# Kernel tuning notes

Hardware: AMD Instinct MI355X
Metric: run time of the kernel (lower is better)

## Reference

```python
import jax, jax.numpy as jnp
import numpy as np

MAX_WORDS = 2048  # max word tokens per sequence (static num_segments)


def setup_inputs() -> dict:
    key = jax.random.key(0)
    k1, k2, k3, k4 = jax.random.split(key, 4)
    B, S, H, D = 8, 4096, 768, 1024
    embeddings = jax.random.normal(k1, (B, S, H), dtype=jnp.float32)
    proj_w = jax.random.normal(k2, (H, D), dtype=jnp.float32) * 0.02
    proj_b = jax.random.normal(k3, (D,), dtype=jnp.float32) * 0.02
    masks = jnp.ones((B, S), dtype=jnp.int32)
    word_ids = jnp.sort(jax.random.randint(k4, (B, S), 0, MAX_WORDS), axis=-1)
    return {"embeddings": embeddings, "proj_w": proj_w, "proj_b": proj_b,
            "masks": masks, "word_ids": word_ids}


def reference(embeddings, proj_w, proj_b, masks, word_ids):
    B, S, H = embeddings.shape
    W = MAX_WORDS
    # Flatten batch+word into one segment id space: seg in [0, B*W)
    seg = (word_ids + jnp.arange(B, dtype=word_ids.dtype)[:, None] * W).reshape(-1)
    flat_emb = embeddings.reshape(B * S, H)
    # segment-sum of embeddings over subwords of each word  -> (B, W, H)
    sum_emb = jax.ops.segment_sum(flat_emb, seg, num_segments=B * W).reshape(B, W, H)
    ones = jnp.ones((B * S,), dtype=jnp.float32)
    counts = jax.ops.segment_sum(ones, seg, num_segments=B * W).reshape(B, W)
    mcounts = jax.ops.segment_sum(masks.reshape(-1).astype(jnp.float32), seg,
                                  num_segments=B * W).reshape(B, W)
    # word is valid iff it has >=1 subword and ALL its subwords have mask==1
    valid = (counts > 0) & (counts == mcounts)
    mean_emb = sum_emb / jnp.maximum(counts, 1.0)[..., None]
    token_embeddings = jnp.where(valid[..., None], mean_emb, 0.0)  # (B, W, H)
    token_masks = valid.astype(jnp.int32)                          # (B, W)
    # projection: hidden 768 -> config.hidden_size 1024
    out = jnp.einsum('bwh,hd->bwd', token_embeddings, proj_w) + proj_b
    return out, token_masks
```

## Files before the change

kernel.cpp:

```cpp
#include <hip/hip_runtime.h>
#include <hip/hip_bf16.h>
#include <stdint.h>

#define Bn 8
#define Sn 4096
#define Hn 768
#define Dn 1024
#define Wn 2048

typedef __attribute__((ext_vector_type(8))) short short8;
typedef __attribute__((ext_vector_type(4))) short short4v;
typedef __attribute__((ext_vector_type(4))) float floatx4;

__device__ __forceinline__ void load_lds16(const void* g, void* l) {
  __builtin_amdgcn_global_load_lds(
      (const __attribute__((address_space(1))) void*)g,
      (__attribute__((address_space(3))) void*)l, 16, 0, 0);
}

__global__ __launch_bounds__(256) void k_prep(const float* __restrict__ pw,
                                              const int* __restrict__ wid,
                                              __hip_bfloat16* __restrict__ wb,
                                              int* __restrict__ starts) {
  if (blockIdx.x < 768) {
    __shared__ float tile[32][33];
    const int bt = blockIdx.x;
    const int d0 = (bt % 32) * 32, h0 = (bt / 32) * 32;
    const int tx = threadIdx.x & 31, ty = threadIdx.x >> 5;
#pragma unroll
    for (int i = 0; i < 32; i += 8)
      tile[ty + i][tx] = pw[(size_t)(h0 + ty + i) * Dn + d0 + tx];
    __syncthreads();
#pragma unroll
    for (int i = 0; i < 32; i += 8)
      wb[(size_t)(d0 + ty + i) * Hn + h0 + tx] = (__hip_bfloat16)tile[tx][ty + i];
  } else {
    const int bid = blockIdx.x - 768;
    const int g = bid * 256 + threadIdx.x;
    const int b = g >> 12, s = g & (Sn - 1);
    const int* wbi = wid + (size_t)b * Sn;
    int* sb = starts + b * (Wn + 1);
    const int cur = wbi[s];
    const int prev = (s == 0) ? -1 : wbi[s - 1];
    for (int ww = prev + 1; ww <= cur; ++ww) sb[ww] = s;
    if (s == Sn - 1)
      for (int ww = cur + 1; ww <= Wn; ++ww) sb[ww] = Sn;
  }
}

__global__ __launch_bounds__(256) void k_words(const float* __restrict__ emb,
                                               const int* __restrict__ masks,
                                               const int* __restrict__ starts,
                                               __hip_bfloat16* __restrict__ wa,
                                               float* __restrict__ out_masks) {
  const int b = blockIdx.y;
  const int wave = threadIdx.x >> 6, lane = threadIdx.x & 63;
  const int w = blockIdx.x * 4 + wave;

  const int* sb = starts + b * (Wn + 1);
  const int start = sb[w];
  const int end = sb[w + 1];
  const int count = end - start;

  const int* mb = masks + (size_t)b * Sn;
  bool allone = true;
  for (int s0 = start; s0 < end; s0 += 64) {
    const int idx = s0 + lane;
    allone = allone && ((idx < end) ? (mb[idx] == 1) : true);
  }
  const bool valid = (count > 0) && __all(allone);
  const float inv = valid ? 1.0f / (float)count : 0.0f;

  floatx4 sum[3] = {{0.f, 0.f, 0.f, 0.f}, {0.f, 0.f, 0.f, 0.f}, {0.f, 0.f, 0.f, 0.f}};
  const float* eb = emb + (size_t)b * Sn * Hn;
  int s = start;
  for (; s + 1 < end; s += 2) {
    const floatx4* r0 = (const floatx4*)(eb + (size_t)s * Hn);
    const floatx4* r1 = (const floatx4*)(eb + (size_t)(s + 1) * Hn);
#pragma unroll
    for (int j = 0; j < 3; ++j) sum[j] += r0[j * 64 + lane];
#pragma unroll
    for (int j = 0; j < 3; ++j) sum[j] += r1[j * 64 + lane];
  }
  if (s < end) {
    const floatx4* r0 = (const floatx4*)(eb + (size_t)s * Hn);
#pragma unroll
    for (int j = 0; j < 3; ++j) sum[j] += r0[j * 64 + lane];
  }

  const size_t rowbase = ((size_t)b * Wn + w) * Hn;
#pragma unroll
  for (int j = 0; j < 3; ++j) {
    short4v o;
#pragma unroll
    for (int c = 0; c < 4; ++c) {
      __hip_bfloat16 h = (__hip_bfloat16)(sum[j][c] * inv);
      o[c] = *reinterpret_cast<short*>(&h);
    }
    *(short4v*)&wa[rowbase + (size_t)(j * 64 + lane) * 4] = o;
  }
  if (lane == 0) out_masks[(size_t)b * Wn + w] = valid ? 1.0f : 0.0f;
}

constexpr int GK = Hn;
constexpr int LDS_A = 256 * 64;
constexpr int LDS_B = 128 * 64;
constexpr int LDS_T = LDS_A + LDS_B;

__global__ __launch_bounds__(512, 2) void k_gemm(const short* __restrict__ A,
                                                 const short* __restrict__ Bt,
                                                 const float* __restrict__ bias,
                                                 float* __restrict__ out) {
  extern __shared__ __align__(16) short ls[];

  const int t = threadIdx.x;
  const int lane = t & 63;
  const int wave = t >> 6;
  const int wm = wave >> 1, wn = wave & 1;
  const int lane16 = lane & 15, quad = lane >> 4;
  const int swz = lane16 & 7;

  const int linear = blockIdx.x;
  const int xcd = linear & 7;
  const int o = linear >> 3;
  const int m0 = (xcd * 8 + (o >> 3)) * 256;
  const int n0 = (o & 7) * 128;

  const int rA = t >> 3;
  const int ssw = ((t & 7) ^ (rA & 7)) * 8;
  const short* gAs = A + (size_t)(m0 + rA) * GK + ssw;
  const short* gBs = Bt + (size_t)(n0 + rA) * GK + ssw;

  auto stage_a3 = [&](int slot, int tt) {
    short* d = ls + slot * LDS_T + t * 8;
    const short* g = gAs + tt * 64;
    load_lds16(g, d);
    load_lds16(g + (size_t)64 * GK, d + 4096);
    load_lds16(g + (size_t)128 * GK, d + 8192);
  };
  auto stage_b3 = [&](int slot, int tt) {
    short* d = ls + slot * LDS_T + t * 8;
    load_lds16(gAs + tt * 64 + (size_t)192 * GK, d + 12288);
    load_lds16(gBs + tt * 64, d + 16384);
    load_lds16(gBs + tt * 64 + (size_t)64 * GK, d + 20480);
  };

  auto ld_af = [&](short8 (&af)[2][2], int mib, const short* bufA) {
#pragma unroll
    for (int m2 = 0; m2 < 2; ++m2)
#pragma unroll
      for (int ks = 0; ks < 2; ++ks)
        af[m2][ks] = *(const short8*)&bufA[(wm * 64 + (mib + m2) * 16 + lane16) * 64 +
                                           ((((ks << 2) | quad) ^ swz) << 3)];
  };
  auto ld_bf = [&](short8 (&bf)[4][2], const short* bufB) {
#pragma unroll
    for (int ni = 0; ni < 4; ++ni)
#pragma unroll
      for (int ks = 0; ks < 2; ++ks)
        bf[ni][ks] = *(const short8*)&bufB[(wn * 64 + ni * 16 + lane16) * 64 +
                                           ((((ks << 2) | quad) ^ swz) << 3)];
  };

  floatx4 acc[4][4];
#pragma unroll
  for (int i = 0; i < 4; ++i)
#pragma unroll
    for (int j = 0; j < 4; ++j) acc[i][j] = (floatx4){0.f, 0.f, 0.f, 0.f};

  auto mmac2 = [&](short8 (&af)[2][2], short8 (&bf)[4][2], int mib) {
    __builtin_amdgcn_s_setprio(1);
#pragma unroll
    for (int m2 = 0; m2 < 2; ++m2)
#pragma unroll
      for (int ni = 0; ni < 4; ++ni)
#pragma unroll
        for (int ks = 0; ks < 2; ++ks)
          acc[mib + m2][ni] = __builtin_amdgcn_mfma_f32_16x16x32_bf16(
              af[m2][ks], bf[ni][ks], acc[mib + m2][ni], 0, 0, 0);
    __builtin_amdgcn_s_setprio(0);
  };

  stage_a3(0, 0);
  stage_b3(0, 0);
  stage_a3(1, 1);
  stage_b3(1, 1);
  asm volatile("s_waitcnt vmcnt(6)" ::: "memory");
  __builtin_amdgcn_sched_barrier(0);
  __builtin_amdgcn_s_barrier();

  int cur = 0;
#pragma unroll 1
  for (int tt = 0; tt < 12; ++tt) {
    const short* bufA = ls + cur * LDS_T;
    const short* bufB = bufA + LDS_A;
    const int nx2 = (cur + 2 >= 3) ? cur - 1 : cur + 2;
    const bool st = tt < 10;
    short8 af[2][2], bf[4][2];

    ld_af(af, 0, bufA);
    ld_bf(bf, bufB);
    if (st) stage_a3(nx2, tt + 2);
    __builtin_amdgcn_s_barrier();
    asm volatile("s_waitcnt lgkmcnt(0)" ::: "memory");
    __builtin_amdgcn_sched_barrier(0);
    mmac2(af, bf, 0);
    __builtin_amdgcn_s_barrier();

    ld_af(af, 2, bufA);
    if (st) stage_b3(nx2, tt + 2);
    if (tt < 10) {
      asm volatile("s_waitcnt vmcnt(6)" ::: "memory");
    } else if (tt == 10) {
      asm volatile("s_waitcnt vmcnt(0)" ::: "memory");
    }
    __builtin_amdgcn_sched_barrier(0);
    __builtin_amdgcn_s_barrier();
    asm volatile("s_waitcnt lgkmcnt(0)" ::: "memory");
    __builtin_amdgcn_sched_barrier(0);
    mmac2(af, bf, 2);
    __builtin_amdgcn_s_barrier();

    cur = (cur + 1 == 3) ? 0 : cur + 1;
  }

  float bv[4];
#pragma unroll
  for (int ni = 0; ni < 4; ++ni) bv[ni] = bias[n0 + wn * 64 + ni * 16 + lane16];

#pragma unroll
  for (int mi = 0; mi < 4; ++mi) {
#pragma unroll
    for (int ni = 0; ni < 4; ++ni) {
      const int n = n0 + wn * 64 + ni * 16 + lane16;
#pragma unroll
      for (int r = 0; r < 4; ++r) {
        const int m = m0 + wm * 64 + mi * 16 + quad * 4 + r;
        out[(size_t)m * Dn + n] = acc[mi][ni][r] + bv[ni];
      }
    }
  }
}

extern "C" void kernel_launch(void* const* d_in, const int* in_sizes, int n_in,
                              void* d_out, int out_size, void* d_ws, size_t ws_size,
                              hipStream_t stream) {
  const float* emb    = (const float*)d_in[0];
  const float* proj_w = (const float*)d_in[1];
  const float* proj_b = (const float*)d_in[2];
  const int*   masks  = (const int*)d_in[3];
  const int*   wid    = (const int*)d_in[4];

  float* out = (float*)d_out;
  float* out_masks = out + (size_t)Bn * Wn * Dn;

  __hip_bfloat16* wb = (__hip_bfloat16*)d_ws;
  __hip_bfloat16* wa = wb + (size_t)Dn * Hn;
  int* starts = (int*)(wa + (size_t)Bn * Wn * Hn);

  k_prep<<<dim3(768 + (Bn * Sn) / 256), 256, 0, stream>>>(proj_w, wid, wb, starts);

  k_words<<<dim3(Wn / 4, Bn), 256, 0, stream>>>(emb, masks, starts, wa, out_masks);

  constexpr int kGemmLds = 3 * LDS_T * (int)sizeof(short);
  static_assert(kGemmLds == 147456, "LDS budget");
  (void)hipFuncSetAttribute((const void*)k_gemm,
                            hipFuncAttributeMaxDynamicSharedMemorySize, kGemmLds);
  k_gemm<<<dim3(512), 512, kGemmLds, stream>>>((const short*)wa, (const short*)wb,
                                               proj_b, out);
}
```

Baseline: 209.9 us.

## Fuse prep, word pooling and GEMM into one cooperative persistent kernel

```diff
diff --git a/kernel.cpp b/kernel.cpp
--- a/kernel.cpp
+++ b/kernel.cpp
@@ -1,6 +1,9 @@
 #include <hip/hip_runtime.h>
+#include <hip/hip_cooperative_groups.h>
 #include <hip/hip_bf16.h>
 #include <stdint.h>
+
+namespace cg = cooperative_groups;
 
 #define Bn 8
 #define Sn 4096
@@ -12,31 +15,47 @@
 typedef __attribute__((ext_vector_type(4))) short short4v;
 typedef __attribute__((ext_vector_type(4))) float floatx4;
 
+constexpr int GK = Hn;
+constexpr int LDS_A = 256 * 64;
+constexpr int LDS_B = 128 * 64;
+constexpr int LDS_T = LDS_A + LDS_B;
+constexpr int kLdsBytes = 3 * LDS_T * (int)sizeof(short);
+static_assert(kLdsBytes == 147456, "LDS budget");
+
 __device__ __forceinline__ void load_lds16(const void* g, void* l) {
   __builtin_amdgcn_global_load_lds(
       (const __attribute__((address_space(1))) void*)g,
       (__attribute__((address_space(3))) void*)l, 16, 0, 0);
 }
 
-__global__ __launch_bounds__(256) void k_prep(const float* __restrict__ pw,
-                                              const int* __restrict__ wid,
-                                              __hip_bfloat16* __restrict__ wb,
-                                              int* __restrict__ starts) {
-  if (blockIdx.x < 768) {
-    __shared__ float tile[32][33];
-    const int bt = blockIdx.x;
-    const int d0 = (bt % 32) * 32, h0 = (bt / 32) * 32;
-    const int tx = threadIdx.x & 31, ty = threadIdx.x >> 5;
-#pragma unroll
-    for (int i = 0; i < 32; i += 8)
-      tile[ty + i][tx] = pw[(size_t)(h0 + ty + i) * Dn + d0 + tx];
-    __syncthreads();
-#pragma unroll
-    for (int i = 0; i < 32; i += 8)
-      wb[(size_t)(d0 + ty + i) * Hn + h0 + tx] = (__hip_bfloat16)tile[tx][ty + i];
+__global__ __launch_bounds__(512, 2) void k_fused(
+    const float* __restrict__ emb, const float* __restrict__ pw,
+    const float* __restrict__ bias, const int* __restrict__ masks,
+    const int* __restrict__ wid, short* wb, short* wa, int* starts,
+    float* __restrict__ out, float* __restrict__ out_masks) {
+  extern __shared__ __align__(16) short ls[];
+  const int t = threadIdx.x;
+  const int bid = blockIdx.x;
+  cg::grid_group grid = cg::this_grid();
+
+  if (bid < 192) {
+    float* tile = (float*)ls;
+    const int tx = t & 31, ty = t >> 5;
+#pragma unroll 1
+    for (int i = 0; i < 4; ++i) {
+      const int bt = bid * 4 + i;
+      const int d0 = (bt & 31) * 32, h0 = (bt >> 5) * 32;
+      tile[ty * 33 + tx] = pw[(size_t)(h0 + ty) * Dn + d0 + tx];
+      tile[(ty + 16) * 33 + tx] = pw[(size_t)(h0 + ty + 16) * Dn + d0 + tx];
+      __syncthreads();
+      __hip_bfloat16 v0 = (__hip_bfloat16)tile[tx * 33 + ty];
+      __hip_bfloat16 v1 = (__hip_bfloat16)tile[tx * 33 + ty + 16];
+      wb[(size_t)(d0 + ty) * Hn + h0 + tx] = *(short*)&v0;
+      wb[(size_t)(d0 + ty + 16) * Hn + h0 + tx] = *(short*)&v1;
+      __syncthreads();
+    }
   } else {
-    const int bid = blockIdx.x - 768;
-    const int g = bid * 256 + threadIdx.x;
+    const int g = (bid - 192) * 512 + t;
     const int b = g >> 12, s = g & (Sn - 1);
     const int* wbi = wid + (size_t)b * Sn;
     int* sb = starts + b * (Wn + 1);
@@ -46,197 +65,197 @@
     if (s == Sn - 1)
       for (int ww = cur + 1; ww <= Wn; ++ww) sb[ww] = Sn;
   }
-}
-
-__global__ __launch_bounds__(256) void k_words(const float* __restrict__ emb,
-                                               const int* __restrict__ masks,
-                                               const int* __restrict__ starts,
-                                               __hip_bfloat16* __restrict__ wa,
-                                               float* __restrict__ out_masks) {
-  const int b = blockIdx.y;
-  const int wave = threadIdx.x >> 6, lane = threadIdx.x & 63;
-  const int w = blockIdx.x * 4 + wave;
-
-  const int* sb = starts + b * (Wn + 1);
-  const int start = sb[w];
-  const int end = sb[w + 1];
-  const int count = end - start;
-
-  const int* mb = masks + (size_t)b * Sn;
-  bool allone = true;
-  for (int s0 = start; s0 < end; s0 += 64) {
-    const int idx = s0 + lane;
-    allone = allone && ((idx < end) ? (mb[idx] == 1) : true);
+  __threadfence();
+  grid.sync();
+
+  {
+    const int wave = t >> 6, lane = t & 63;
+    const int gw0 = (bid * 8 + wave) * 8;
+    const int b = gw0 >> 11;
+    const int w0 = gw0 & (Wn - 1);
+    const int* sb = starts + b * (Wn + 1);
+    const int pre = (lane < 9) ? sb[w0 + lane] : 0;
+    const int* mb = masks + (size_t)b * Sn;
+    const float* eb = emb + (size_t)b * Sn * Hn;
+
+    for (int wi = 0; wi < 8; ++wi) {
+      const int start = __shfl(pre, wi);
+      const int end = __shfl(pre, wi + 1);
+      const int count = end - start;
+
+      bool allone = true;
+      for (int s0 = start; s0 < end; s0 += 64) {
+        const int idx = s0 + lane;
+        allone = allone && ((idx < end) ? (mb[idx] == 1) : true);
+      }
+      const bool valid = (count > 0) && __all(allone);
+      const float inv = valid ? 1.0f / (float)count : 0.0f;
+
+      floatx4 sum[3] = {{0.f, 0.f, 0.f, 0.f}, {0.f, 0.f, 0.f, 0.f},
+                        {0.f, 0.f, 0.f, 0.f}};
+      int s = start;
+      for (; s + 1 < end; s += 2) {
+        const floatx4* r0 = (const floatx4*)(eb + (size_t)s * Hn);
+        const floatx4* r1 = (const floatx4*)(eb + (size_t)(s + 1) * Hn);
+#pragma unroll
+        for (int j = 0; j < 3; ++j) sum[j] += r0[j * 64 + lane];
+#pragma unroll
+        for (int j = 0; j < 3; ++j) sum[j] += r1[j * 64 + lane];
+      }
+      if (s < end) {
+        const floatx4* r0 = (const floatx4*)(eb + (size_t)s * Hn);
+#pragma unroll
+        for (int j = 0; j < 3; ++j) sum[j] += r0[j * 64 + lane];
+      }
+
+      const int w = w0 + wi;
+      const size_t rowbase = ((size_t)b * Wn + w) * Hn;
+#pragma unroll
+      for (int j = 0; j < 3; ++j) {
+        short4v o;
+#pragma unroll
+        for (int c = 0; c < 4; ++c) {
+          __hip_bfloat16 h = (__hip_bfloat16)(sum[j][c] * inv);
+          o[c] = *reinterpret_cast<short*>(&h);
+        }
+        *(short4v*)&wa[rowbase + (size_t)(j * 64 + lane) * 4] = o;
+      }
+      if (lane == 0) out_masks[(size_t)b * Wn + w] = valid ? 1.0f : 0.0f;
+    }
   }
-  const bool valid = (count > 0) && __all(allone);
-  const float inv = valid ? 1.0f / (float)count : 0.0f;
-
-  floatx4 sum[3] = {{0.f, 0.f, 0.f, 0.f}, {0.f, 0.f, 0.f, 0.f}, {0.f, 0.f, 0.f, 0.f}};
-  const float* eb = emb + (size_t)b * Sn * Hn;
-  int s = start;
-  for (; s + 1 < end; s += 2) {
-    const floatx4* r0 = (const floatx4*)(eb + (size_t)s * Hn);
-    const floatx4* r1 = (const floatx4*)(eb + (size_t)(s + 1) * Hn);
-#pragma unroll
-    for (int j = 0; j < 3; ++j) sum[j] += r0[j * 64 + lane];
-#pragma unroll
-    for (int j = 0; j < 3; ++j) sum[j] += r1[j * 64 + lane];
-  }
-  if (s < end) {
-    const floatx4* r0 = (const floatx4*)(eb + (size_t)s * Hn);
-#pragma unroll
-    for (int j = 0; j < 3; ++j) sum[j] += r0[j * 64 + lane];
-  }
-
-  const size_t rowbase = ((size_t)b * Wn + w) * Hn;
-#pragma unroll
-  for (int j = 0; j < 3; ++j) {
-    short4v o;
-#pragma unroll
-    for (int c = 0; c < 4; ++c) {
-      __hip_bfloat16 h = (__hip_bfloat16)(sum[j][c] * inv);
-      o[c] = *reinterpret_cast<short*>(&h);
-    }
-    *(short4v*)&wa[rowbase + (size_t)(j * 64 + lane) * 4] = o;
-  }
-  if (lane == 0) out_masks[(size_t)b * Wn + w] = valid ? 1.0f : 0.0f;
-}
-
-constexpr int GK = Hn;
-constexpr int LDS_A = 256 * 64;
-constexpr int LDS_B = 128 * 64;
-constexpr int LDS_T = LDS_A + LDS_B;
-
-__global__ __launch_bounds__(512, 2) void k_gemm(const short* __restrict__ A,
-                                                 const short* __restrict__ Bt,
-                                                 const float* __restrict__ bias,
-                                                 float* __restrict__ out) {
-  extern __shared__ __align__(16) short ls[];
-
-  const int t = threadIdx.x;
-  const int lane = t & 63;
-  const int wave = t >> 6;
-  const int wm = wave >> 1, wn = wave & 1;
-  const int lane16 = lane & 15, quad = lane >> 4;
-  const int swz = lane16 & 7;
-
-  const int linear = blockIdx.x;
-  const int xcd = linear & 7;
-  const int o = linear >> 3;
-  const int m0 = (xcd * 8 + (o >> 3)) * 256;
-  const int n0 = (o & 7) * 128;
-
-  const int rA = t >> 3;
-  const int ssw = ((t & 7) ^ (rA & 7)) * 8;
-  const short* gAs = A + (size_t)(m0 + rA) * GK + ssw;
-  const short* gBs = Bt + (size_t)(n0 + rA) * GK + ssw;
-
-  auto stage_a3 = [&](int slot, int tt) {
-    short* d = ls + slot * LDS_T + t * 8;
-    const short* g = gAs + tt * 64;
-    load_lds16(g, d);
-    load_lds16(g + (size_t)64 * GK, d + 4096);
-    load_lds16(g + (size_t)128 * GK, d + 8192);
-  };
-  auto stage_b3 = [&](int slot, int tt) {
-    short* d = ls + slot * LDS_T + t * 8;
-    load_lds16(gAs + tt * 64 + (size_t)192 * GK, d + 12288);
-    load_lds16(gBs + tt * 64, d + 16384);
-    load_lds16(gBs + tt * 64 + (size_t)64 * GK, d + 20480);
-  };
-
-  auto ld_af = [&](short8 (&af)[2][2], int mib, const short* bufA) {
-#pragma unroll
-    for (int m2 = 0; m2 < 2; ++m2)
-#pragma unroll
-      for (int ks = 0; ks < 2; ++ks)
-        af[m2][ks] = *(const short8*)&bufA[(wm * 64 + (mib + m2) * 16 + lane16) * 64 +
-                                           ((((ks << 2) | quad) ^ swz) << 3)];
-  };
-  auto ld_bf = [&](short8 (&bf)[4][2], const short* bufB) {
-#pragma unroll
-    for (int ni = 0; ni < 4; ++ni)
-#pragma unroll
-      for (int ks = 0; ks < 2; ++ks)
-        bf[ni][ks] = *(const short8*)&bufB[(wn * 64 + ni * 16 + lane16) * 64 +
-                                           ((((ks << 2) | quad) ^ swz) << 3)];
-  };
-
-  floatx4 acc[4][4];
-#pragma unroll
-  for (int i = 0; i < 4; ++i)
-#pragma unroll
-    for (int j = 0; j < 4; ++j) acc[i][j] = (floatx4){0.f, 0.f, 0.f, 0.f};
-
-  auto mmac2 = [&](short8 (&af)[2][2], short8 (&bf)[4][2], int mib) {
-    __builtin_amdgcn_s_setprio(1);
-#pragma unroll
-    for (int m2 = 0; m2 < 2; ++m2)
+  __threadfence();
+  grid.sync();
+
+  {
+    const int lane = t & 63, wave = t >> 6;
+    const int wm = wave >> 1, wn = wave & 1;
+    const int lane16 = lane & 15, quad = lane >> 4;
+    const int swz = lane16 & 7;
+
+    const int xcd = bid & 7, o = bid >> 3;
+    const int m0 = (xcd * 8 + (o >> 2)) * 256;
+    const int n0b = (o & 3) * 256;
+
+    const int rA = t >> 3;
+    const int ssw = ((t & 7) ^ (rA & 7)) * 8;
+    const short* gAs = (const short*)wa + (size_t)(m0 + rA) * GK + ssw;
+
+#pragma unroll 1
+    for (int nt = 0; nt < 2; ++nt) {
+      const int n0 = n0b + nt * 128;
+      const short* gBs = (const short*)wb + (size_t)(n0 + rA) * GK + ssw;
+
+      auto stage_a3 = [&](int slot, int tt) {
+        short* d = ls + slot * LDS_T + t * 8;
+        const short* g = gAs + tt * 64;
+        load_lds16(g, d);
+        load_lds16(g + (size_t)64 * GK, d + 4096);
+        load_lds16(g + (size_t)128 * GK, d + 8192);
+      };
+      auto stage_b3 = [&](int slot, int tt) {
+        short* d = ls + slot * LDS_T + t * 8;
+        load_lds16(gAs + tt * 64 + (size_t)192 * GK, d + 12288);
+        load_lds16(gBs + tt * 64, d + 16384);
+        load_lds16(gBs + tt * 64 + (size_t)64 * GK, d + 20480);
+      };
+      auto ld_af = [&](short8(&af)[2][2], int mib, const short* bufA) {
+#pragma unroll
+        for (int m2 = 0; m2 < 2; ++m2)
+#pragma unroll
+          for (int ks = 0; ks < 2; ++ks)
+            af[m2][ks] = *(const short8*)&bufA[(wm * 64 + (mib + m2) * 16 + lane16) * 64 +
+                                               ((((ks << 2) | quad) ^ swz) << 3)];
+      };
+      auto ld_bf = [&](short8(&bf)[4][2], const short* bufB) {
+#pragma unroll
+        for (int ni = 0; ni < 4; ++ni)
+#pragma unroll
+          for (int ks = 0; ks < 2; ++ks)
+            bf[ni][ks] = *(const short8*)&bufB[(wn * 64 + ni * 16 + lane16) * 64 +
+                                               ((((ks << 2) | quad) ^ swz) << 3)];
+      };
+
+      floatx4 acc[4][4];
+#pragma unroll
+      for (int i = 0; i < 4; ++i)
+#pragma unroll
+        for (int j = 0; j < 4; ++j) acc[i][j] = (floatx4){0.f, 0.f, 0.f, 0.f};
+
+      auto mmac2 = [&](short8(&af)[2][2], short8(&bf)[4][2], int mib) {
+        __builtin_amdgcn_s_setprio(1);
+#pragma unroll
+        for (int m2 = 0; m2 < 2; ++m2)
+#pragma unroll
+          for (int ni = 0; ni < 4; ++ni)
+#pragma unroll
+            for (int ks = 0; ks < 2; ++ks)
+              acc[mib + m2][ni] = __builtin_amdgcn_mfma_f32_16x16x32_bf16(
+                  af[m2][ks], bf[ni][ks], acc[mib + m2][ni], 0, 0, 0);
+        __builtin_amdgcn_s_setprio(0);
+      };
+
+      asm volatile("s_waitcnt vmcnt(0)" ::: "memory");
+      __builtin_amdgcn_sched_barrier(0);
+
+      stage_a3(0, 0);
+      stage_b3(0, 0);
+      stage_a3(1, 1);
+      stage_b3(1, 1);
+      asm volatile("s_waitcnt vmcnt(6)" ::: "memory");
+      __builtin_amdgcn_sched_barrier(0);
+      __builtin_amdgcn_s_barrier();
+
+      int cur = 0;
+#pragma unroll 1
+      for (int tt = 0; tt < 12; ++tt) {
+        const short* bufA = ls + cur * LDS_T;
+        const short* bufB = bufA + LDS_A;
+        const int nx2 = (cur + 2 >= 3) ? cur - 1 : cur + 2;
+        const bool st = tt < 10;
+        short8 af[2][2], bf[4][2];
+
+        ld_af(af, 0, bufA);
+        ld_bf(bf, bufB);
+        if (st) stage_a3(nx2, tt + 2);
+        __builtin_amdgcn_s_barrier();
+        asm volatile("s_waitcnt lgkmcnt(0)" ::: "memory");
+        __builtin_amdgcn_sched_barrier(0);
+        mmac2(af, bf, 0);
+        __builtin_amdgcn_s_barrier();
+
+        ld_af(af, 2, bufA);
+        if (st) stage_b3(nx2, tt + 2);
+        if (tt < 10) {
+          asm volatile("s_waitcnt vmcnt(6)" ::: "memory");
+        } else if (tt == 10) {
+          asm volatile("s_waitcnt vmcnt(0)" ::: "memory");
+        }
+        __builtin_amdgcn_sched_barrier(0);
+        __builtin_amdgcn_s_barrier();
+        asm volatile("s_waitcnt lgkmcnt(0)" ::: "memory");
+        __builtin_amdgcn_sched_barrier(0);
+        mmac2(af, bf, 2);
+        __builtin_amdgcn_s_barrier();
+
+        cur = (cur + 1 == 3) ? 0 : cur + 1;
+      }
+
+      float bv[4];
 #pragma unroll
       for (int ni = 0; ni < 4; ++ni)
-#pragma unroll
-        for (int ks = 0; ks < 2; ++ks)
-          acc[mib + m2][ni] = __builtin_amdgcn_mfma_f32_16x16x32_bf16(
-              af[m2][ks], bf[ni][ks], acc[mib + m2][ni], 0, 0, 0);
-    __builtin_amdgcn_s_setprio(0);
-  };
-
-  stage_a3(0, 0);
-  stage_b3(0, 0);
-  stage_a3(1, 1);
-  stage_b3(1, 1);
-  asm volatile("s_waitcnt vmcnt(6)" ::: "memory");
-  __builtin_amdgcn_sched_barrier(0);
-  __builtin_amdgcn_s_barrier();
-
-  int cur = 0;
-#pragma unroll 1
-  for (int tt = 0; tt < 12; ++tt) {
-    const short* bufA = ls + cur * LDS_T;
-    const short* bufB = bufA + LDS_A;
-    const int nx2 = (cur + 2 >= 3) ? cur - 1 : cur + 2;
-    const bool st = tt < 10;
-    short8 af[2][2], bf[4][2];
-
-    ld_af(af, 0, bufA);
-    ld_bf(bf, bufB);
-    if (st) stage_a3(nx2, tt + 2);
-    __builtin_amdgcn_s_barrier();
-    asm volatile("s_waitcnt lgkmcnt(0)" ::: "memory");
-    __builtin_amdgcn_sched_barrier(0);
-    mmac2(af, bf, 0);
-    __builtin_amdgcn_s_barrier();
-
-    ld_af(af, 2, bufA);
-    if (st) stage_b3(nx2, tt + 2);
-    if (tt < 10) {
-      asm volatile("s_waitcnt vmcnt(6)" ::: "memory");
-    } else if (tt == 10) {
-      asm volatile("s_waitcnt vmcnt(0)" ::: "memory");
-    }
-    __builtin_amdgcn_sched_barrier(0);
-    __builtin_amdgcn_s_barrier();
-    asm volatile("s_waitcnt lgkmcnt(0)" ::: "memory");
-    __builtin_amdgcn_sched_barrier(0);
-    mmac2(af, bf, 2);
-    __builtin_amdgcn_s_barrier();
-
-    cur = (cur + 1 == 3) ? 0 : cur + 1;
-  }
-
-  float bv[4];
-#pragma unroll
-  for (int ni = 0; ni < 4; ++ni) bv[ni] = bias[n0 + wn * 64 + ni * 16 + lane16];
-
-#pragma unroll
-  for (int mi = 0; mi < 4; ++mi) {
-#pragma unroll
-    for (int ni = 0; ni < 4; ++ni) {
-      const int n = n0 + wn * 64 + ni * 16 + lane16;
-#pragma unroll
-      for (int r = 0; r < 4; ++r) {
-        const int m = m0 + wm * 64 + mi * 16 + quad * 4 + r;
-        out[(size_t)m * Dn + n] = acc[mi][ni][r] + bv[ni];
+        bv[ni] = bias[n0 + wn * 64 + ni * 16 + lane16];
+
+#pragma unroll
+      for (int mi = 0; mi < 4; ++mi) {
+#pragma unroll
+        for (int ni = 0; ni < 4; ++ni) {
+          const int n = n0 + wn * 64 + ni * 16 + lane16;
+#pragma unroll
+          for (int r = 0; r < 4; ++r) {
+            const int m = m0 + wm * 64 + mi * 16 + quad * 4 + r;
+            out[(size_t)m * Dn + n] = acc[mi][ni][r] + bv[ni];
+          }
+        }
       }
     }
   }
@@ -254,18 +273,16 @@
   float* out = (float*)d_out;
   float* out_masks = out + (size_t)Bn * Wn * Dn;
 
-  __hip_bfloat16* wb = (__hip_bfloat16*)d_ws;
-  __hip_bfloat16* wa = wb + (size_t)Dn * Hn;
+  short* wb = (short*)d_ws;
+  short* wa = wb + (size_t)Dn * Hn;
   int* starts = (int*)(wa + (size_t)Bn * Wn * Hn);
 
-  k_prep<<<dim3(768 + (Bn * Sn) / 256), 256, 0, stream>>>(proj_w, wid, wb, starts);
-
-  k_words<<<dim3(Wn / 4, Bn), 256, 0, stream>>>(emb, masks, starts, wa, out_masks);
-
-  constexpr int kGemmLds = 3 * LDS_T * (int)sizeof(short);
-  static_assert(kGemmLds == 147456, "LDS budget");
-  (void)hipFuncSetAttribute((const void*)k_gemm,
-                            hipFuncAttributeMaxDynamicSharedMemorySize, kGemmLds);
-  k_gemm<<<dim3(512), 512, kGemmLds, stream>>>((const short*)wa, (const short*)wb,
-                                               proj_b, out);
+  (void)hipFuncSetAttribute((const void*)k_fused,
+                            hipFuncAttributeMaxDynamicSharedMemorySize, kLdsBytes);
+
+  void* args[] = {(void*)&emb, (void*)&proj_w, (void*)&proj_b, (void*)&masks,
+                  (void*)&wid, (void*)&wb,     (void*)&wa,     (void*)&starts,
+                  (void*)&out, (void*)&out_masks};
+  (void)hipLaunchCooperativeKernel((const void*)k_fused, dim3(256), dim3(512),
+                                   args, kLdsBytes, stream);
 }
```

Measured after the change: 414.6 us. 1.98x slower.
